# Optimization experiments

Hardware: AMD Instinct MI355X
Metric: run time of the kernel (lower is better)

Reference implementation:

```python
import jax, jax.numpy as jnp
import numpy as np

ALPHA = 0.2  # LeakyReLU negative slope
MASK_FILL = -9e15


def setup_inputs() -> dict:
    key = jax.random.key(0)
    k_x, k_adj, k_W, k_a = jax.random.split(key, 4)
    B, N, Fin, T, O = 8, 1024, 64, 8, 128
    x = jax.random.normal(k_x, (B, N, Fin, T), dtype=jnp.float32)
    adj = (jax.random.uniform(k_adj, (N, N)) < 0.05).astype(jnp.float32)
    adj = jnp.maximum(adj, jnp.eye(N, dtype=jnp.float32))
    W = jax.random.normal(k_W, (Fin, O), dtype=jnp.float32) * (1.414 * (6.0 / (Fin + O)) ** 0.5)
    a = jax.random.normal(k_a, (2 * O, 1), dtype=jnp.float32) * (1.414 * (6.0 / (2 * O + 1)) ** 0.5)
    return {"x": x, "adj": adj, "W": W, "a": a}


def reference(x, adj, W, a):
    # x: (B, N, Fin, T), adj: (N, N), W: (Fin, O), a: (2O, 1)
    O = W.shape[1]
    xt = jnp.transpose(x, (0, 3, 1, 2))                 # (B, T, N, Fin)
    Wh = jnp.einsum('btnf,fo->btno', xt, W)             # (B, T, N, O)
    a1 = a[:O, 0]                                       # (O,)
    a2 = a[O:, 0]                                       # (O,)
    Wh1 = Wh @ a1                                       # (B, T, N)
    Wh2 = Wh @ a2                                       # (B, T, N)
    e = Wh1[..., :, None] + Wh2[..., None, :]           # (B, T, N, N): e_ij = Wh1_i + Wh2_j
    e = jax.nn.leaky_relu(e, negative_slope=ALPHA)
    e = jnp.where(adj > 0, e, MASK_FILL)
    attn = jax.nn.softmax(e, axis=-1)                   # softmax over neighbors j (torch dim=1 on (N,N))
    # dropout on attention is identity at inference (training=False)
    h_prime = jnp.einsum('btij,btjo->btio', attn, Wh)   # (B, T, N, O)
    out = jnp.transpose(h_prime, (0, 2, 3, 1))          # (B, N, O, T)
    return jax.nn.elu(out)                              # concat=True -> ELU
```

## Files before the change

kernel.cpp:

```cpp
#include <hip/hip_runtime.h>
#include <math.h>
#include <stdint.h>

#define ALPHA 0.2f

typedef __attribute__((ext_vector_type(8))) short bf16x8;
typedef __attribute__((ext_vector_type(4))) float f32x4;

__global__ __launch_bounds__(512) void k_wh(const float* __restrict__ x,
                                            const float* __restrict__ W,
                                            const float* __restrict__ a,
                                            uint4* __restrict__ Whf,
                                            float* __restrict__ Wh1,
                                            float* __restrict__ Wh2) {
    __shared__ float xs[32 * 512];
    __shared__ float Wv[8 * 16 * 68];

    const int tid = threadIdx.x;
    const int b   = blockIdx.x & 7;
    const int jt  = blockIdx.x >> 3;

    const float4* xg4 = (const float4*)(x + ((size_t)(b * 1024 + jt * 32)) * 512);
    #pragma unroll
    for (int i = 0; i < 8; ++i) {
        int    idx = tid + i * 512;
        float4 v   = xg4[idx];
        int jl  = idx >> 7;
        int rem = idx & 127;
        int f   = rem >> 1;
        int tq  = rem & 1;
        int kk  = f ^ ((jl >> 3) << 2);
        float* dst = &xs[jl * 512 + (tq * 4) * 64 + kk];
        dst[0]   = v.x;
        dst[64]  = v.y;
        dst[128] = v.z;
        dst[192] = v.w;
    }
    const float4* Wg4 = (const float4*)W;
    #pragma unroll
    for (int i = 0; i < 4; ++i) {
        int    idx = tid + i * 512;
        float4 v   = Wg4[idx];
        int k  = idx >> 5;
        int o0 = (idx & 31) * 4;
        #pragma unroll
        for (int c = 0; c < 4; ++c) {
            int o = o0 + c;
            Wv[o * 68 + k] = (&v.x)[c];
        }
    }
    __syncthreads();

    const int w  = tid >> 6;
    const int l  = tid & 63;
    const int q  = l >> 4;
    const int om = l & 15;
    const int t  = w;

    float acc[8][8];
    #pragma unroll
    for (int jj = 0; jj < 8; ++jj)
        #pragma unroll
        for (int nt = 0; nt < 8; ++nt) acc[jj][nt] = 0.f;

    for (int kc = 0; kc < 64; kc += 4) {
        float4 xv[8], wv[8];
        const int kx = kc ^ (q << 2);
        #pragma unroll
        for (int jj = 0; jj < 8; ++jj)
            xv[jj] = *(const float4*)&xs[(q * 8 + jj) * 512 + t * 64 + kx];
        #pragma unroll
        for (int nt = 0; nt < 8; ++nt)
            wv[nt] = *(const float4*)&Wv[(nt * 16 + om) * 68 + kc];
        #pragma unroll
        for (int jj = 0; jj < 8; ++jj) {
            #pragma unroll
            for (int nt = 0; nt < 8; ++nt) {
                float s = acc[jj][nt];
                s = fmaf(xv[jj].x, wv[nt].x, s);
                s = fmaf(xv[jj].y, wv[nt].y, s);
                s = fmaf(xv[jj].z, wv[nt].z, s);
                s = fmaf(xv[jj].w, wv[nt].w, s);
                acc[jj][nt] = s;
            }
        }
    }

    const int bt = b * 8 + t;

    float a1v[8], a2v[8];
    #pragma unroll
    for (int nt = 0; nt < 8; ++nt) {
        a1v[nt] = a[nt * 16 + om];
        a2v[nt] = a[128 + nt * 16 + om];
    }
    #pragma unroll
    for (int jj = 0; jj < 8; ++jj) {
        float s1 = 0.f, s2 = 0.f;
        #pragma unroll
        for (int nt = 0; nt < 8; ++nt) {
            s1 = fmaf(acc[jj][nt], a1v[nt], s1);
            s2 = fmaf(acc[jj][nt], a2v[nt], s2);
        }
        #pragma unroll
        for (int off = 1; off < 16; off <<= 1) {
            s1 += __shfl_xor(s1, off);
            s2 += __shfl_xor(s2, off);
        }
        if (om == 0) {
            int j = jt * 32 + q * 8 + jj;
            Wh1[bt * 1024 + j] = s1;
            Wh2[bt * 1024 + j] = s2;
        }
    }

    #pragma unroll
    for (int nt = 0; nt < 8; ++nt) {
        uint32_t u[4];
        #pragma unroll
        for (int pr = 0; pr < 4; ++pr) {
            uint32_t lo = (__float_as_uint(acc[2 * pr][nt]) + 0x8000u) >> 16;
            uint32_t hi = (__float_as_uint(acc[2 * pr + 1][nt]) + 0x8000u) & 0xFFFF0000u;
            u[pr] = lo | hi;
        }
        uint4 st; st.x = u[0]; st.y = u[1]; st.z = u[2]; st.w = u[3];
        Whf[((size_t)(bt * 32 + jt) * 8 + nt) * 64 + l] = st;
    }
}

__global__ __launch_bounds__(256) void k_adjb(const float* __restrict__ adj,
                                              unsigned char* __restrict__ adjb) {
    int idx = blockIdx.x * 256 + threadIdx.x;
    const float4* a4 = (const float4*)adj + idx * 2;
    float4 v0 = a4[0], v1 = a4[1];
    unsigned int by = 0;
    by |= (v0.x > 0.f) ? 1u : 0u;
    by |= (v0.y > 0.f) ? 2u : 0u;
    by |= (v0.z > 0.f) ? 4u : 0u;
    by |= (v0.w > 0.f) ? 8u : 0u;
    by |= (v1.x > 0.f) ? 16u : 0u;
    by |= (v1.y > 0.f) ? 32u : 0u;
    by |= (v1.z > 0.f) ? 64u : 0u;
    by |= (v1.w > 0.f) ? 128u : 0u;
    adjb[idx] = (unsigned char)by;
}

__global__ __launch_bounds__(256) void k_agg(const uint4* __restrict__ Whf,
                                             const float* __restrict__ Wh1,
                                             const float* __restrict__ Wh2,
                                             const unsigned char* __restrict__ adjb,
                                             float* __restrict__ out) {
    __shared__ float        wh2s[1024];
    __shared__ unsigned int adjs_u[128 * 33];
    __shared__ float        wh1s[128];
    __shared__ float        lls[128];
    __shared__ float        m2s[4];

    const int tid   = threadIdx.x;
    const int b     = blockIdx.x & 7;
    const int t     = (blockIdx.x >> 3) & 7;
    const int itile = blockIdx.x >> 6;
    const int bt    = b * 8 + t;
    const int i0    = itile * 128;

    const float* wh2g = Wh2 + bt * 1024;
    for (int i = tid; i < 1024; i += 256) wh2s[i] = wh2g[i];
    if (tid < 128) wh1s[tid] = Wh1[bt * 1024 + i0 + tid];
    const unsigned int* adjg_u = (const unsigned int*)(adjb + i0 * 128);
    for (int idx = tid; idx < 4096; idx += 256)
        adjs_u[(idx >> 5) * 33 + (idx & 31)] = adjg_u[idx];
    __syncthreads();

    const int w = tid >> 6;
    const int l = tid & 63;
    const int q = l >> 4;
    const int m = l & 15;

    float mx = fmaxf(fmaxf(wh2s[w * 256 + l], wh2s[w * 256 + 64 + l]),
                     fmaxf(wh2s[w * 256 + 128 + l], wh2s[w * 256 + 192 + l]));
    #pragma unroll
    for (int off = 1; off < 64; off <<= 1) mx = fmaxf(mx, __shfl_xor(mx, off));
    if (l == 0) m2s[w] = mx;
    __syncthreads();
    const float M2 = fmaxf(fmaxf(m2s[0], m2s[1]), fmaxf(m2s[2], m2s[3]));

    float wh1v[2], mc[2];
    #pragma unroll
    for (int ms = 0; ms < 2; ++ms) {
        float h1 = wh1s[w * 32 + ms * 16 + m];
        float e  = h1 + M2;
        wh1v[ms] = h1;
        mc[ms]   = fmaxf(e, ALPHA * e);
    }

    f32x4 acc[2][8];
    #pragma unroll
    for (int ms = 0; ms < 2; ++ms)
        #pragma unroll
        for (int nt = 0; nt < 8; ++nt) { acc[ms][nt] = (f32x4){0.f, 0.f, 0.f, 0.f}; }
    float lacc[2] = {0.f, 0.f};

    const uint4*         bfg  = Whf + (size_t)bt * 32 * 8 * 64 + l;
    const unsigned char* adjs = (const unsigned char*)adjs_u;
    const int            arow = (w * 32 + m) * 132;

    for (int s = 0; s < 32; ++s) {
        union { float4 f4[2]; float f[8]; } w2;
        w2.f4[0] = *(const float4*)&wh2s[s * 32 + q * 8];
        w2.f4[1] = *(const float4*)&wh2s[s * 32 + q * 8 + 4];
        unsigned int byv[2];
        byv[0] = adjs[arow + s * 4 + q];
        byv[1] = adjs[arow + 16 * 132 + s * 4 + q];

        bf16x8 afr[2];
        #pragma unroll
        for (int ms = 0; ms < 2; ++ms) {
            const float h1 = wh1v[ms], mp = mc[ms];
            const unsigned int by = byv[ms];
            uint32_t ub[8];
            float    ls = 0.f;
            #pragma unroll
            for (int jj = 0; jj < 8; ++jj) {
                float e   = h1 + w2.f[jj];
                float lr  = fmaxf(e, ALPHA * e);
                float arg = ((by >> jj) & 1u) ? (lr - mp) : -1e30f;
                float p   = __expf(arg);
                uint32_t r = (__float_as_uint(p) + 0x8000u) >> 16;
                ub[jj] = r;
                ls += __uint_as_float(r << 16);
            }
            union { uint32_t u[4]; bf16x8 v; } pk;
            #pragma unroll
            for (int pr = 0; pr < 4; ++pr)
                pk.u[pr] = ub[2 * pr] | (ub[2 * pr + 1] << 16);
            afr[ms] = pk.v;
            lacc[ms] += ls;
        }

        const uint4* bp = bfg + (size_t)s * 8 * 64;
        #pragma unroll
        for (int nt = 0; nt < 8; ++nt) {
            union { uint4 u; bf16x8 v; } br;
            br.u = bp[nt * 64];
            acc[0][nt] = __builtin_amdgcn_mfma_f32_16x16x32_bf16(afr[0], br.v, acc[0][nt], 0, 0, 0);
            acc[1][nt] = __builtin_amdgcn_mfma_f32_16x16x32_bf16(afr[1], br.v, acc[1][nt], 0, 0, 0);
        }
    }

    #pragma unroll
    for (int ms = 0; ms < 2; ++ms) {
        lacc[ms] += __shfl_xor(lacc[ms], 16);
        lacc[ms] += __shfl_xor(lacc[ms], 32);
    }
    if (q == 0) {
        lls[w * 32 + m]      = lacc[0];
        lls[w * 32 + 16 + m] = lacc[1];
    }
    __syncthreads();

    float* og = out + ((size_t)(b * 1024 + i0 + w * 32)) * 1024 + t;
    #pragma unroll
    for (int ms = 0; ms < 2; ++ms) {
        #pragma unroll
        for (int reg = 0; reg < 4; ++reg) {
            int   row  = ms * 16 + q * 4 + reg;
            float linv = 1.0f / lls[w * 32 + row];
            #pragma unroll
            for (int nt = 0; nt < 8; ++nt) {
                float v = acc[ms][nt][reg] * linv;
                v = v > 0.f ? v : __expf(v) - 1.f;
                og[(size_t)row * 1024 + (nt * 16 + m) * 8] = v;
            }
        }
    }
}

extern "C" void kernel_launch(void* const* d_in, const int* in_sizes, int n_in,
                              void* d_out, int out_size, void* d_ws, size_t ws_size,
                              hipStream_t stream) {
    const float* x   = (const float*)d_in[0];
    const float* adj = (const float*)d_in[1];
    const float* W   = (const float*)d_in[2];
    const float* a   = (const float*)d_in[3];
    float* out = (float*)d_out;

    uint4*         Whf  = (uint4*)d_ws;
    float*         Wh1  = (float*)(Whf + 1048576);
    float*         Wh2  = Wh1 + 65536;
    unsigned char* adjb = (unsigned char*)(Wh2 + 65536);

    k_wh  <<<256, 512, 0, stream>>>(x, W, a, Whf, Wh1, Wh2);
    k_adjb<<<512, 256, 0, stream>>>(adj, adjb);
    k_agg <<<512, 256, 0, stream>>>(Whf, Wh1, Wh2, adjb, out);
}
```

Before: 151.3 us.

## Factor attention exponentials, halve Wh tiles, widen aggregation blocks, MFMA row sums

The attention exponential is factored as exp(lr(h1+h2)-m) = A*exp(h2) or B*exp(alpha*h2), with both exp terms for each neighbour precomputed once per block. This removes the per-element __expf from the inner aggregation loop. The row sums are now produced by an extra MFMA against a ones vector instead of scalar accumulation and a shuffle reduction. k_wh processes 16 rows per block (twice the blocks) with a swizzled W layout to cut LDS bank conflicts, and k_agg uses 8 waves of 16 rows each; the trade is possible overflow or underflow of exp(h2) and exp(-h1) for large-magnitude logits.

```diff
diff --git a/kernel.cpp b/kernel.cpp
--- a/kernel.cpp
+++ b/kernel.cpp
@@ -7,29 +7,34 @@
 typedef __attribute__((ext_vector_type(8))) short bf16x8;
 typedef __attribute__((ext_vector_type(4))) float f32x4;
 
-__global__ __launch_bounds__(512) void k_wh(const float* __restrict__ x,
-                                            const float* __restrict__ W,
-                                            const float* __restrict__ a,
-                                            uint4* __restrict__ Whf,
-                                            float* __restrict__ Wh1,
-                                            float* __restrict__ Wh2) {
-    __shared__ float xs[32 * 512];
-    __shared__ float Wv[8 * 16 * 68];
+__device__ __forceinline__ uint32_t pack_bf16(float a, float b) {
+    return ((__float_as_uint(a) + 0x8000u) >> 16) |
+           ((__float_as_uint(b) + 0x8000u) & 0xFFFF0000u);
+}
+
+__global__ __launch_bounds__(512, 4) void k_wh(const float* __restrict__ x,
+                                               const float* __restrict__ W,
+                                               const float* __restrict__ a,
+                                               uint4* __restrict__ Whf,
+                                               float* __restrict__ Wh1,
+                                               float* __restrict__ Wh2) {
+    __shared__ float xs[16 * 512];
+    __shared__ float Wv[128 * 68];
 
     const int tid = threadIdx.x;
     const int b   = blockIdx.x & 7;
     const int jt  = blockIdx.x >> 3;
 
-    const float4* xg4 = (const float4*)(x + ((size_t)(b * 1024 + jt * 32)) * 512);
-    #pragma unroll
-    for (int i = 0; i < 8; ++i) {
+    const float4* xg4 = (const float4*)(x + (size_t)(b * 1024 + jt * 16) * 512);
+    #pragma unroll
+    for (int i = 0; i < 4; ++i) {
         int    idx = tid + i * 512;
         float4 v   = xg4[idx];
         int jl  = idx >> 7;
         int rem = idx & 127;
         int f   = rem >> 1;
         int tq  = rem & 1;
-        int kk  = f ^ ((jl >> 3) << 2);
+        int kk  = f ^ ((jl >> 2) << 2);
         float* dst = &xs[jl * 512 + (tq * 4) * 64 + kk];
         dst[0]   = v.x;
         dst[64]  = v.y;
@@ -45,8 +50,9 @@
         int o0 = (idx & 31) * 4;
         #pragma unroll
         for (int c = 0; c < 4; ++c) {
-            int o = o0 + c;
-            Wv[o * 68 + k] = (&v.x)[c];
+            int o   = o0 + c;
+            int adr = o * 68 + ((((k >> 2) ^ ((o >> 3) & 7)) << 2) | (k & 3));
+            Wv[adr] = (&v.x)[c];
         }
     }
     __syncthreads();
@@ -57,23 +63,26 @@
     const int om = l & 15;
     const int t  = w;
 
-    float acc[8][8];
-    #pragma unroll
-    for (int jj = 0; jj < 8; ++jj)
+    float acc[4][8];
+    #pragma unroll
+    for (int jj = 0; jj < 4; ++jj)
         #pragma unroll
         for (int nt = 0; nt < 8; ++nt) acc[jj][nt] = 0.f;
 
     for (int kc = 0; kc < 64; kc += 4) {
-        float4 xv[8], wv[8];
+        float4 xv[4], wv[8];
         const int kx = kc ^ (q << 2);
         #pragma unroll
-        for (int jj = 0; jj < 8; ++jj)
-            xv[jj] = *(const float4*)&xs[(q * 8 + jj) * 512 + t * 64 + kx];
-        #pragma unroll
-        for (int nt = 0; nt < 8; ++nt)
-            wv[nt] = *(const float4*)&Wv[(nt * 16 + om) * 68 + kc];
-        #pragma unroll
-        for (int jj = 0; jj < 8; ++jj) {
+        for (int jj = 0; jj < 4; ++jj)
+            xv[jj] = *(const float4*)&xs[(q * 4 + jj) * 512 + t * 64 + kx];
+        #pragma unroll
+        for (int nt = 0; nt < 8; ++nt) {
+            int og  = nt * 16 + om;
+            int grp = (kc >> 2) ^ ((nt * 2 + (om >> 3)) & 7);
+            wv[nt]  = *(const float4*)&Wv[og * 68 + grp * 4];
+        }
+        #pragma unroll
+        for (int jj = 0; jj < 4; ++jj) {
             #pragma unroll
             for (int nt = 0; nt < 8; ++nt) {
                 float s = acc[jj][nt];
@@ -95,7 +104,7 @@
         a2v[nt] = a[128 + nt * 16 + om];
     }
     #pragma unroll
-    for (int jj = 0; jj < 8; ++jj) {
+    for (int jj = 0; jj < 4; ++jj) {
         float s1 = 0.f, s2 = 0.f;
         #pragma unroll
         for (int nt = 0; nt < 8; ++nt) {
@@ -108,23 +117,22 @@
             s2 += __shfl_xor(s2, off);
         }
         if (om == 0) {
-            int j = jt * 32 + q * 8 + jj;
+            int j = jt * 16 + q * 4 + jj;
             Wh1[bt * 1024 + j] = s1;
             Wh2[bt * 1024 + j] = s2;
         }
     }
 
+    const int    q8l   = ((jt & 1) << 1) | (q >> 1);
+    const int    l8    = (q8l << 4) | om;
+    const size_t fbase = (size_t)(bt * 32 + (jt >> 1)) * 8;
     #pragma unroll
     for (int nt = 0; nt < 8; ++nt) {
-        uint32_t u[4];
-        #pragma unroll
-        for (int pr = 0; pr < 4; ++pr) {
-            uint32_t lo = (__float_as_uint(acc[2 * pr][nt]) + 0x8000u) >> 16;
-            uint32_t hi = (__float_as_uint(acc[2 * pr + 1][nt]) + 0x8000u) & 0xFFFF0000u;
-            u[pr] = lo | hi;
-        }
-        uint4 st; st.x = u[0]; st.y = u[1]; st.z = u[2]; st.w = u[3];
-        Whf[((size_t)(bt * 32 + jt) * 8 + nt) * 64 + l] = st;
+        uint2 st;
+        st.x = pack_bf16(acc[0][nt], acc[1][nt]);
+        st.y = pack_bf16(acc[2][nt], acc[3][nt]);
+        char* p = (char*)(Whf + (fbase + nt) * 64 + l8) + ((q & 1) << 3);
+        *(uint2*)p = st;
     }
 }
 
@@ -145,16 +153,15 @@
     adjb[idx] = (unsigned char)by;
 }
 
-__global__ __launch_bounds__(256) void k_agg(const uint4* __restrict__ Whf,
-                                             const float* __restrict__ Wh1,
-                                             const float* __restrict__ Wh2,
-                                             const unsigned char* __restrict__ adjb,
-                                             float* __restrict__ out) {
-    __shared__ float        wh2s[1024];
+__global__ __launch_bounds__(512, 4) void k_agg(const uint4* __restrict__ Whf,
+                                                const float* __restrict__ Wh1,
+                                                const float* __restrict__ Wh2,
+                                                const unsigned char* __restrict__ adjb,
+                                                float* __restrict__ out) {
+    __shared__ __attribute__((aligned(16))) float2 efs[1024];
     __shared__ unsigned int adjs_u[128 * 33];
-    __shared__ float        wh1s[128];
-    __shared__ float        lls[128];
-    __shared__ float        m2s[4];
+    __shared__ float wh1s[128];
+    __shared__ float m2s[8];
 
     const int tid   = threadIdx.x;
     const int b     = blockIdx.x & 7;
@@ -163,114 +170,100 @@
     const int bt    = b * 8 + t;
     const int i0    = itile * 128;
 
-    const float* wh2g = Wh2 + bt * 1024;
-    for (int i = tid; i < 1024; i += 256) wh2s[i] = wh2g[i];
-    if (tid < 128) wh1s[tid] = Wh1[bt * 1024 + i0 + tid];
-    const unsigned int* adjg_u = (const unsigned int*)(adjb + i0 * 128);
-    for (int idx = tid; idx < 4096; idx += 256)
-        adjs_u[(idx >> 5) * 33 + (idx & 31)] = adjg_u[idx];
-    __syncthreads();
-
     const int w = tid >> 6;
     const int l = tid & 63;
     const int q = l >> 4;
     const int m = l & 15;
 
-    float mx = fmaxf(fmaxf(wh2s[w * 256 + l], wh2s[w * 256 + 64 + l]),
-                     fmaxf(wh2s[w * 256 + 128 + l], wh2s[w * 256 + 192 + l]));
+    const float* wh2g = Wh2 + bt * 1024;
+    float mx = -1e30f;
+    for (int j = tid; j < 1024; j += 512) {
+        float h2 = wh2g[j];
+        float2 ef;
+        ef.x = __expf(h2);
+        ef.y = __expf(ALPHA * h2);
+        efs[j] = ef;
+        mx = fmaxf(mx, h2);
+    }
     #pragma unroll
     for (int off = 1; off < 64; off <<= 1) mx = fmaxf(mx, __shfl_xor(mx, off));
     if (l == 0) m2s[w] = mx;
+    if (tid < 128) wh1s[tid] = Wh1[bt * 1024 + i0 + tid];
+    const unsigned int* adjg = (const unsigned int*)(adjb + i0 * 128);
+    for (int idx = tid; idx < 4096; idx += 512)
+        adjs_u[(idx >> 5) * 33 + (idx & 31)] = adjg[idx];
     __syncthreads();
-    const float M2 = fmaxf(fmaxf(m2s[0], m2s[1]), fmaxf(m2s[2], m2s[3]));
-
-    float wh1v[2], mc[2];
-    #pragma unroll
-    for (int ms = 0; ms < 2; ++ms) {
-        float h1 = wh1s[w * 32 + ms * 16 + m];
-        float e  = h1 + M2;
-        wh1v[ms] = h1;
-        mc[ms]   = fmaxf(e, ALPHA * e);
-    }
-
-    f32x4 acc[2][8];
-    #pragma unroll
-    for (int ms = 0; ms < 2; ++ms)
-        #pragma unroll
-        for (int nt = 0; nt < 8; ++nt) { acc[ms][nt] = (f32x4){0.f, 0.f, 0.f, 0.f}; }
-    float lacc[2] = {0.f, 0.f};
-
-    const uint4*         bfg  = Whf + (size_t)bt * 32 * 8 * 64 + l;
-    const unsigned char* adjs = (const unsigned char*)adjs_u;
-    const int            arow = (w * 32 + m) * 132;
+
+    float M2 = m2s[0];
+    #pragma unroll
+    for (int i = 1; i < 8; ++i) M2 = fmaxf(M2, m2s[i]);
+
+    const int   row = w * 16 + m;
+    const float h1  = wh1s[row];
+    const float e0  = h1 + M2;
+    const float mp  = fmaxf(e0, ALPHA * e0);
+    const float Af  = __expf(h1 - mp);
+    const float Bf  = __expf(ALPHA * h1 - mp);
+    const float G   = __expf(-h1);
+
+    f32x4 acc[8];
+    #pragma unroll
+    for (int nt = 0; nt < 8; ++nt) acc[nt] = (f32x4){0.f, 0.f, 0.f, 0.f};
+    f32x4 accl = (f32x4){0.f, 0.f, 0.f, 0.f};
+
+    bf16x8 ones;
+    #pragma unroll
+    for (int i = 0; i < 8; ++i) ones[i] = (short)0x3F80;
+
+    const uint4* bfg = Whf + (size_t)bt * 32 * 8 * 64 + l;
 
     for (int s = 0; s < 32; ++s) {
-        union { float4 f4[2]; float f[8]; } w2;
-        w2.f4[0] = *(const float4*)&wh2s[s * 32 + q * 8];
-        w2.f4[1] = *(const float4*)&wh2s[s * 32 + q * 8 + 4];
-        unsigned int byv[2];
-        byv[0] = adjs[arow + s * 4 + q];
-        byv[1] = adjs[arow + 16 * 132 + s * 4 + q];
-
-        bf16x8 afr[2];
-        #pragma unroll
-        for (int ms = 0; ms < 2; ++ms) {
-            const float h1 = wh1v[ms], mp = mc[ms];
-            const unsigned int by = byv[ms];
-            uint32_t ub[8];
-            float    ls = 0.f;
-            #pragma unroll
-            for (int jj = 0; jj < 8; ++jj) {
-                float e   = h1 + w2.f[jj];
-                float lr  = fmaxf(e, ALPHA * e);
-                float arg = ((by >> jj) & 1u) ? (lr - mp) : -1e30f;
-                float p   = __expf(arg);
-                uint32_t r = (__float_as_uint(p) + 0x8000u) >> 16;
-                ub[jj] = r;
-                ls += __uint_as_float(r << 16);
-            }
-            union { uint32_t u[4]; bf16x8 v; } pk;
-            #pragma unroll
-            for (int pr = 0; pr < 4; ++pr)
-                pk.u[pr] = ub[2 * pr] | (ub[2 * pr + 1] << 16);
-            afr[ms] = pk.v;
-            lacc[ms] += ls;
-        }
+        const float* eb = (const float*)&efs[s * 32 + q * 8];
+        float4 ef01 = *(const float4*)(eb + 0);
+        float4 ef23 = *(const float4*)(eb + 4);
+        float4 ef45 = *(const float4*)(eb + 8);
+        float4 ef67 = *(const float4*)(eb + 12);
+        const unsigned int dw = adjs_u[row * 33 + s];
+
+        float E[8], F[8];
+        E[0] = ef01.x; F[0] = ef01.y; E[1] = ef01.z; F[1] = ef01.w;
+        E[2] = ef23.x; F[2] = ef23.y; E[3] = ef23.z; F[3] = ef23.w;
+        E[4] = ef45.x; F[4] = ef45.y; E[5] = ef45.z; F[5] = ef45.w;
+        E[6] = ef67.x; F[6] = ef67.y; E[7] = ef67.z; F[7] = ef67.w;
+
+        float p[8];
+        #pragma unroll
+        for (int jj = 0; jj < 8; ++jj) {
+            bool  cond = E[jj] > G;
+            float pr   = (cond ? Af : Bf) * (cond ? E[jj] : F[jj]);
+            p[jj] = ((dw >> (q * 8 + jj)) & 1u) ? pr : 0.0f;
+        }
+
+        union { uint32_t u[4]; bf16x8 v; } pk;
+        #pragma unroll
+        for (int pr2 = 0; pr2 < 4; ++pr2)
+            pk.u[pr2] = pack_bf16(p[2 * pr2], p[2 * pr2 + 1]);
 
         const uint4* bp = bfg + (size_t)s * 8 * 64;
         #pragma unroll
         for (int nt = 0; nt < 8; ++nt) {
             union { uint4 u; bf16x8 v; } br;
             br.u = bp[nt * 64];
-            acc[0][nt] = __builtin_amdgcn_mfma_f32_16x16x32_bf16(afr[0], br.v, acc[0][nt], 0, 0, 0);
-            acc[1][nt] = __builtin_amdgcn_mfma_f32_16x16x32_bf16(afr[1], br.v, acc[1][nt], 0, 0, 0);
-        }
-    }
-
-    #pragma unroll
-    for (int ms = 0; ms < 2; ++ms) {
-        lacc[ms] += __shfl_xor(lacc[ms], 16);
-        lacc[ms] += __shfl_xor(lacc[ms], 32);
-    }
-    if (q == 0) {
-        lls[w * 32 + m]      = lacc[0];
-        lls[w * 32 + 16 + m] = lacc[1];
-    }
-    __syncthreads();
-
-    float* og = out + ((size_t)(b * 1024 + i0 + w * 32)) * 1024 + t;
-    #pragma unroll
-    for (int ms = 0; ms < 2; ++ms) {
-        #pragma unroll
-        for (int reg = 0; reg < 4; ++reg) {
-            int   row  = ms * 16 + q * 4 + reg;
-            float linv = 1.0f / lls[w * 32 + row];
-            #pragma unroll
-            for (int nt = 0; nt < 8; ++nt) {
-                float v = acc[ms][nt][reg] * linv;
-                v = v > 0.f ? v : __expf(v) - 1.f;
-                og[(size_t)row * 1024 + (nt * 16 + m) * 8] = v;
-            }
+            acc[nt] = __builtin_amdgcn_mfma_f32_16x16x32_bf16(pk.v, br.v, acc[nt], 0, 0, 0);
+        }
+        accl = __builtin_amdgcn_mfma_f32_16x16x32_bf16(pk.v, ones, accl, 0, 0, 0);
+    }
+
+    float* og = out + ((size_t)(b * 1024 + i0 + w * 16)) * 1024 + t;
+    #pragma unroll
+    for (int reg = 0; reg < 4; ++reg) {
+        const int   r    = q * 4 + reg;
+        const float linv = 1.0f / accl[reg];
+        #pragma unroll
+        for (int nt = 0; nt < 8; ++nt) {
+            float v = acc[nt][reg] * linv;
+            v = v > 0.f ? v : __expf(v) - 1.f;
+            og[(size_t)r * 1024 + (nt * 16 + m) * 8] = v;
         }
     }
 }
@@ -289,7 +282,7 @@
     float*         Wh2  = Wh1 + 65536;
     unsigned char* adjb = (unsigned char*)(Wh2 + 65536);
 
-    k_wh  <<<256, 512, 0, stream>>>(x, W, a, Whf, Wh1, Wh2);
+    k_wh  <<<512, 512, 0, stream>>>(x, W, a, Whf, Wh1, Wh2);
     k_adjb<<<512, 256, 0, stream>>>(adj, adjb);
-    k_agg <<<512, 256, 0, stream>>>(Whf, Wh1, Wh2, adjb, out);
-}
+    k_agg <<<512, 512, 0, stream>>>(Whf, Wh1, Wh2, adjb, out);
+}
```

After: 159.8 us. 1.06x slower.
